# Optimization experiments

Measured on AMD Instinct MI355X. Metric: run time of the kernel, lower is better.

The kernel has to match this reference:

```python
import jax, jax.numpy as jnp
import numpy as np
import math

B, S, HID, L, NH, V, M = 8, 512, 768, 12, 12, 30522, 512
FF = 4 * HID
D = HID // NH


def sinusoidal_pe(seq_len, dim):
    pos = np.arange(seq_len, dtype=np.float32)[:, None]
    i = np.arange(dim // 2, dtype=np.float32)[None, :]
    ang = pos / np.power(10000.0, 2.0 * i / dim)
    pe = np.zeros((seq_len, dim), np.float32)
    pe[:, 0::2] = np.sin(ang)
    pe[:, 1::2] = np.cos(ang)
    return jnp.asarray(pe)


def setup_inputs() -> dict:
    key = jax.random.key(0)
    ks = iter(jax.random.split(key, 32))
    g = lambda sh: jax.random.normal(next(ks), sh, jnp.float32) * 0.02
    return {
        "token_ids": jax.random.randint(next(ks), (B, S), 0, V),
        "segment_info": jax.random.randint(next(ks), (B, S), 0, 2),
        "tok_emb": g((V, HID)),
        "seg_emb": g((3, HID)),
        "Wq": g((L, HID, HID)), "bq": jnp.zeros((L, HID)),
        "Wk": g((L, HID, HID)), "bk": jnp.zeros((L, HID)),
        "Wv": g((L, HID, HID)), "bv": jnp.zeros((L, HID)),
        "Wo": g((L, HID, HID)), "bo": jnp.zeros((L, HID)),
        "Wpk": g((L, HID, HID)),
        "Wpq": g((L, HID, HID)),
        "rel_emb": g((L, 2 * M, HID)),
        "ln1_g": jnp.ones((L, HID)), "ln1_b": jnp.zeros((L, HID)),
        "ln2_g": jnp.ones((L, HID)), "ln2_b": jnp.zeros((L, HID)),
        "W1": g((L, HID, FF)), "b1": jnp.zeros((L, FF)),
        "W2": g((L, FF, HID)), "b2": jnp.zeros((L, HID)),
        "lnf_g": jnp.ones((HID,)), "lnf_b": jnp.zeros((HID,)),
    }


def _ln(x, g, b):
    mu = x.mean(-1, keepdims=True)
    var = ((x - mu) ** 2).mean(-1, keepdims=True)
    return (x - mu) * jax.lax.rsqrt(var + 1e-5) * g + b


def _forward(token_ids, segment_info, tok_emb, seg_emb, layer_params, lnf_g, lnf_b):
    mask = token_ids != 0  # [B,S] valid-key mask
    x = tok_emb[token_ids] + sinusoidal_pe(S, HID)[None] + seg_emb[segment_info]
    qidx = jnp.arange(S)[:, None]
    # relative position bucket: clamp(q-k, -M, M-1) + M  -> [0, 2M)
    rel = jnp.clip(qidx - jnp.arange(S)[None, :], -M, M - 1) + M  # [S,S]
    scale = 1.0 / math.sqrt(3.0 * D)  # DeBERTa scales by sqrt(3d) for 3 score terms

    def body(x, p):
        (Wq, bq, Wk, bk, Wv, bv, Wo, bo, Wpk, Wpq, rel_e,
         l1g, l1b, l2g, l2b, W1, b1, W2, b2) = p
        # pre-norm attention sublayer
        h = _ln(x, l1g, l1b)
        q = (h @ Wq + bq).reshape(B, S, NH, D)
        k = (h @ Wk + bk).reshape(B, S, NH, D)
        v = (h @ Wv + bv).reshape(B, S, NH, D)
        c2c = jnp.einsum('bqhd,bkhd->bhqk', q, k)
        pk = (rel_e @ Wpk).reshape(2 * M, NH, D)
        pq = (rel_e @ Wpq).reshape(2 * M, NH, D)
        # content-to-position: Q_q . posK[rel(q,k)]
        c2p = jnp.einsum('bqhd,rhd->bhqr', q, pk)[:, :, qidx, rel]  # [B,NH,S,S]
        # position-to-content: K_k . posQ[rel(k,q)] -> gather over k rows then transpose
        p2c = jnp.einsum('bkhd,rhd->bhkr', k, pq)[:, :, qidx, rel]  # [B,NH,k,q]
        scores = (c2c + c2p + jnp.swapaxes(p2c, -1, -2)) * scale
        scores = jnp.where(mask[:, None, None, :], scores, -1e9)
        attn = jax.nn.softmax(scores, axis=-1)
        ctx = jnp.einsum('bhqk,bkhd->bqhd', attn, v).reshape(B, S, HID)
        x = x + ctx @ Wo + bo
        # pre-norm feedforward sublayer
        h2 = _ln(x, l2g, l2b)
        x = x + jax.nn.gelu(h2 @ W1 + b1, approximate=False) @ W2 + b2
        return x, None

    x, _ = jax.lax.scan(body, x, layer_params)
    return _ln(x, lnf_g, lnf_b)


def reference(token_ids, segment_info, tok_emb, seg_emb, Wq, bq, Wk, bk, Wv, bv,
              Wo, bo, Wpk, Wpq, rel_emb, ln1_g, ln1_b, ln2_g, ln2_b,
              W1, b1, W2, b2, lnf_g, lnf_b):
    lp = (Wq, bq, Wk, bk, Wv, bv, Wo, bo, Wpk, Wpq, rel_emb,
          ln1_g, ln1_b, ln2_g, ln2_b, W1, b1, W2, b2)
    return _forward(token_ids, segment_info, tok_emb, seg_emb, lp, lnf_g, lnf_b)
```

## Files before the change

### kernel.cpp

```cpp
#include <hip/hip_runtime.h>
#include <hip/hip_bf16.h>
#include <cstddef>
#include <cstdint>


constexpr int B   = 8;
constexpr int S   = 512;
constexpr int HID = 768;
constexpr int L   = 12;
constexpr int NH  = 12;
constexpr int D   = 64;
constexpr int FF  = 3072;
constexpr int M2  = 1024;
constexpr int NTOK = B * S;

using f32x4 = __attribute__((ext_vector_type(4))) float;
using s16x8 = __attribute__((ext_vector_type(8))) short;

__device__ inline float wave_sum(float v) {
#pragma unroll
  for (int o = 32; o > 0; o >>= 1) v += __shfl_xor(v, o, 64);
  return v;
}
__device__ inline unsigned short f2bf(float f) {
  __hip_bfloat16 h = __float2bfloat16(f);
  return *reinterpret_cast<unsigned short*>(&h);
}
__device__ inline float bf2f(unsigned short u) {
  union { unsigned int i; float f; } x;
  x.i = ((unsigned int)u) << 16;
  return x.f;
}
#define GLOAD16(gp, lp)                                                  \
  __builtin_amdgcn_global_load_lds(                                     \
      (const __attribute__((address_space(1))) void*)(gp),              \
      (__attribute__((address_space(3))) void*)(lp), 16, 0, 0)

__global__ void embed_kernel(const int* __restrict__ tok,
                             const int* __restrict__ seg,
                             const float* __restrict__ tok_emb,
                             const float* __restrict__ seg_emb,
                             float* __restrict__ x) {
  int row = blockIdx.x;
  int s = row & (S - 1);
  int t = tok[row];
  int sg = seg[row];
  for (int c = threadIdx.x; c < HID; c += blockDim.x) {
    int i = c >> 1;
    float ang = (float)s * powf(10000.0f, -2.0f * (float)i / (float)HID);
    float pe = (c & 1) ? cosf(ang) : sinf(ang);
    x[(size_t)row * HID + c] = tok_emb[(size_t)t * HID + c] + pe
                             + seg_emb[(size_t)sg * HID + c];
  }
}

template <int BF16OUT>
__global__ __launch_bounds__(256)
void ln_kernel(const float* __restrict__ in, void* __restrict__ outp,
               const float* __restrict__ g, const float* __restrict__ b,
               int nrows) {
  int wave = threadIdx.x >> 6, lane = threadIdx.x & 63;
  int row = blockIdx.x * 4 + wave;
  if (row >= nrows) return;
  const float* xr = in + (size_t)row * HID;
  float v[12];
  float s = 0.f;
#pragma unroll
  for (int i = 0; i < 12; i++) { v[i] = xr[lane + i * 64]; s += v[i]; }
  s = wave_sum(s);
  float mu = s * (1.0f / HID);
  float ss = 0.f;
#pragma unroll
  for (int i = 0; i < 12; i++) { float d = v[i] - mu; ss += d * d; }
  ss = wave_sum(ss);
  float inv = rsqrtf(ss * (1.0f / HID) + 1e-5f);
#pragma unroll
  for (int i = 0; i < 12; i++) {
    int c = lane + i * 64;
    float o = (v[i] - mu) * inv * g[c] + b[c];
    if (BF16OUT)
      ((unsigned short*)outp)[(size_t)row * HID + c] = f2bf(o);
    else
      ((float*)outp)[(size_t)row * HID + c] = o;
  }
}

__global__ __launch_bounds__(256)
void transpose_kernel(const float* __restrict__ src,
                      unsigned short* __restrict__ dst, int K, int N) {
  __shared__ float tile[32][33];
  int nt = blockIdx.x * 32, kt = blockIdx.y * 32;
  int tx = threadIdx.x & 31, ty = threadIdx.x >> 5;
#pragma unroll
  for (int i = 0; i < 4; i++)
    tile[ty + i * 8][tx] = src[(size_t)(kt + ty + i * 8) * N + nt + tx];
  __syncthreads();
#pragma unroll
  for (int i = 0; i < 4; i++)
    dst[(size_t)(nt + ty + i * 8) * K + kt + tx] = f2bf(tile[tx][ty + i * 8]);
}

__global__ __launch_bounds__(256)
void transpose6_kernel(const float* s0, const float* s1, const float* s2,
                       const float* s3, const float* s4, const float* s5,
                       unsigned short* __restrict__ dst) {
  const float* srcs[6] = {s0, s1, s2, s3, s4, s5};
  const float* src = srcs[blockIdx.z];
  unsigned short* d = dst + (size_t)blockIdx.z * HID * HID;
  __shared__ float tile[32][33];
  int nt = blockIdx.x * 32, kt = blockIdx.y * 32;
  int tx = threadIdx.x & 31, ty = threadIdx.x >> 5;
#pragma unroll
  for (int i = 0; i < 4; i++)
    tile[ty + i * 8][tx] = src[(size_t)(kt + ty + i * 8) * HID + nt + tx];
  __syncthreads();
#pragma unroll
  for (int i = 0; i < 4; i++)
    d[(size_t)(nt + ty + i * 8) * HID + kt + tx] = f2bf(tile[tx][ty + i * 8]);
}

__global__ void conv_bf16_kernel(const float* __restrict__ src,
                                 unsigned short* __restrict__ dst, int n) {
  int i = blockIdx.x * 256 + threadIdx.x;
  if (i < n) dst[i] = f2bf(src[i]);
}

__global__ void concat_bias(const float* __restrict__ bq,
                            const float* __restrict__ bk,
                            const float* __restrict__ bv,
                            float* __restrict__ bqkv) {
  int i = blockIdx.x * 256 + threadIdx.x;
  if (i >= L * 2304) return;
  int l = i / 2304, c = i % 2304;
  float v = (c < 768) ? bq[l * 768 + c]
          : (c < 1536) ? bk[l * 768 + c - 768] : bv[l * 768 + c - 1536];
  bqkv[i] = v;
}

template <int TN, int OUT_BF16, int GELU, int PARTIAL>
__global__ __launch_bounds__(256)
void mfma_gemm(const unsigned short* __restrict__ A,
               const unsigned short* __restrict__ Bt,
               const float* __restrict__ bias, const float* __restrict__ res,
               void* __restrict__ C, int Mr, int K, int N, int Kc) {
  constexpr int NW = TN / 32;
  __shared__ unsigned short As[128 * 32];
  __shared__ unsigned short Bs[TN * 32];
  int t = threadIdx.x, wave = t >> 6, lane = t & 63;
  int r0 = blockIdx.y * 128, n0 = blockIdx.x * TN;
  int kb = blockIdx.z * Kc;
  int wr = (wave >> 1) * 64;
  int wc = (wave & 1) * (TN / 2);

  f32x4 acc[4][NW] = {};
  int srow = lane >> 2, selem = (lane & 3) * 8;

  for (int k0 = kb; k0 < kb + Kc; k0 += 32) {
    __syncthreads();
    {
      const unsigned short* gA =
          A + (size_t)(r0 + wave * 32 + srow) * K + k0 + selem;
      unsigned short* lA = &As[(wave * 32) * 32];
      GLOAD16(gA, lA);
      GLOAD16(gA + (size_t)16 * K, lA + 16 * 32);
      if (TN == 128) {
        const unsigned short* gB =
            Bt + (size_t)(n0 + wave * 32 + srow) * K + k0 + selem;
        unsigned short* lB = &Bs[(wave * 32) * 32];
        GLOAD16(gB, lB);
        GLOAD16(gB + (size_t)16 * K, lB + 16 * 32);
      } else {
        const unsigned short* gB =
            Bt + (size_t)(n0 + wave * 16 + srow) * K + k0 + selem;
        GLOAD16(gB, &Bs[(wave * 16) * 32]);
      }
    }
    __syncthreads();

    s16x8 af[4], bf[NW];
#pragma unroll
    for (int m = 0; m < 4; m++)
      af[m] = *(const s16x8*)&As[(wr + m * 16 + (lane & 15)) * 32 + (lane >> 4) * 8];
#pragma unroll
    for (int n = 0; n < NW; n++)
      bf[n] = *(const s16x8*)&Bs[(wc + n * 16 + (lane & 15)) * 32 + (lane >> 4) * 8];
#pragma unroll
    for (int m = 0; m < 4; m++)
#pragma unroll
      for (int n = 0; n < NW; n++)
        acc[m][n] = __builtin_amdgcn_mfma_f32_16x16x32_bf16(af[m], bf[n],
                                                            acc[m][n], 0, 0, 0);
  }

  if (PARTIAL) {
    float* Cp = (float*)C + (size_t)blockIdx.z * Mr * N;
#pragma unroll
    for (int n = 0; n < NW; n++) {
      int c = n0 + wc + n * 16 + (lane & 15);
#pragma unroll
      for (int m = 0; m < 4; m++) {
        int rb = r0 + wr + m * 16 + ((lane >> 4) << 2);
#pragma unroll
        for (int j = 0; j < 4; j++)
          Cp[(size_t)(rb + j) * N + c] = acc[m][n][j];
      }
    }
    return;
  }
#pragma unroll
  for (int n = 0; n < NW; n++) {
    int c = n0 + wc + n * 16 + (lane & 15);
    float bv = bias ? bias[c] : 0.f;
#pragma unroll
    for (int m = 0; m < 4; m++) {
      int rb = r0 + wr + m * 16 + ((lane >> 4) << 2);
#pragma unroll
      for (int j = 0; j < 4; j++) {
        int r = rb + j;
        float val = acc[m][n][j] + bv;
        if (GELU) val = 0.5f * val * (1.0f + erff(val * 0.70710678118654752f));
        if (res)  val += res[(size_t)r * N + c];
        if (OUT_BF16)
          ((unsigned short*)C)[(size_t)r * N + c] = f2bf(val);
        else
          ((float*)C)[(size_t)r * N + c] = val;
      }
    }
  }
}

template <int LAST>
__global__ __launch_bounds__(256)
void combine_ln(const float* __restrict__ part,
                float* __restrict__ x, const float* __restrict__ bias,
                const float* __restrict__ g, const float* __restrict__ bb,
                void* __restrict__ outp) {
  int row = blockIdx.x, t = threadIdx.x;
  int wave = t >> 6, lane = t & 63;
  __shared__ float red[4];
  float v[3];
  float s = 0.f;
#pragma unroll
  for (int i = 0; i < 3; i++) {
    int c = t + i * 256;
    size_t idx = (size_t)row * HID + c;
    float val = x[idx] + part[idx] + part[(size_t)NTOK * HID + idx] + bias[c];
    if (!LAST) x[idx] = val;
    v[i] = val;
    s += val;
  }
  s = wave_sum(s);
  if (lane == 0) red[wave] = s;
  __syncthreads();
  float mu = (red[0] + red[1] + red[2] + red[3]) * (1.0f / HID);
  float ss = 0.f;
#pragma unroll
  for (int i = 0; i < 3; i++) { float d = v[i] - mu; ss += d * d; }
  ss = wave_sum(ss);
  __syncthreads();
  if (lane == 0) red[wave] = ss;
  __syncthreads();
  float inv = rsqrtf((red[0] + red[1] + red[2] + red[3]) * (1.0f / HID) + 1e-5f);
#pragma unroll
  for (int i = 0; i < 3; i++) {
    int c = t + i * 256;
    float o = (v[i] - mu) * inv * g[c] + bb[c];
    if (LAST)
      ((float*)outp)[(size_t)row * HID + c] = o;
    else
      ((unsigned short*)outp)[(size_t)row * HID + c] = f2bf(o);
  }
}

__global__ __launch_bounds__(256)
void transpose_v(const unsigned short* __restrict__ qkv,
                 unsigned short* __restrict__ vt) {
  __shared__ unsigned short tile[32][34];
  int bh = blockIdx.z;
  int b = bh / NH, h = bh % NH;
  int s0 = blockIdx.x * 32, d0 = blockIdx.y * 32;
  int tx = threadIdx.x & 31, ty = threadIdx.x >> 5;
#pragma unroll
  for (int i = 0; i < 4; i++)
    tile[ty + i * 8][tx] =
        qkv[(size_t)(b * S + s0 + ty + i * 8) * 2304 + 1536 + h * 64 + d0 + tx];
  __syncthreads();
#pragma unroll
  for (int i = 0; i < 4; i++)
    vt[((size_t)bh * 64 + d0 + ty + i * 8) * S + s0 + tx] = tile[tx][ty + i * 8];
}

__global__ __launch_bounds__(256)
void flash_attn(const unsigned short* __restrict__ qkv,
                const unsigned short* __restrict__ pkq,
                const unsigned short* __restrict__ vt,
                const int* __restrict__ tok,
                unsigned short* __restrict__ ctx) {
  constexpr int RS = 72, TS = 130;
  __shared__ unsigned short Qs[64 * RS];
  __shared__ unsigned short KPs[64 * RS];
  __shared__ unsigned short Vs[64 * RS];
  __shared__ unsigned short Band[2 * 128 * RS];
  __shared__ int smTok[64];
  unsigned short* PKb = Band;
  unsigned short* PQb = Band + 128 * RS;
  unsigned short* c2pL = Band;
  unsigned short* p2cL = Band + 64 * TS;

  int t = threadIdx.x, wave = t >> 6, lane = t & 63;
  int bh = blockIdx.y;
  int b = bh / NH, h = bh % NH;
  int q0 = blockIdx.x * 64;
  int l15 = lane & 15, l4 = lane >> 4;

#pragma unroll
  for (int i = 0; i < 2; i++) {
    int c = t + i * 256;
    int r = c >> 3, d0 = (c & 7) * 8;
    *(s16x8*)&Qs[r * RS + d0] =
        *(const s16x8*)&qkv[(size_t)(b * S + q0 + r) * 2304 + h * 64 + d0];
  }

  float m[4], l[4];
  f32x4 accO[4];
#pragma unroll
  for (int j = 0; j < 4; j++) { m[j] = -1e30f; l[j] = 0.f; }
#pragma unroll
  for (int n = 0; n < 4; n++) accO[n] = (f32x4){0.f, 0.f, 0.f, 0.f};

  const float scale = 0.07216878364870323f;

  for (int k0 = 0; k0 < S; k0 += 64) {
#pragma unroll
    for (int i = 0; i < 2; i++) {
      int c = t + i * 256;
      int r = c >> 3, d0 = (c & 7) * 8;
      *(s16x8*)&KPs[r * RS + d0] =
          *(const s16x8*)&qkv[(size_t)(b * S + k0 + r) * 2304 + 768 + h * 64 + d0];
      *(s16x8*)&Vs[r * RS + d0] =
          *(const s16x8*)&vt[((size_t)bh * 64 + r) * S + k0 + d0];
    }
    int lo1 = q0 - k0 + 449;
    int lo2 = k0 - q0 + 449;
#pragma unroll
    for (int i = 0; i < 4; i++) {
      int c = t + i * 256;
      int tt = c >> 3, d0 = (c & 7) * 8;
      int r1 = lo1 + tt; r1 = r1 < 0 ? 0 : (r1 > M2 - 1 ? M2 - 1 : r1);
      int r2 = lo2 + tt; r2 = r2 < 0 ? 0 : (r2 > M2 - 1 ? M2 - 1 : r2);
      *(s16x8*)&PKb[tt * RS + d0] = *(const s16x8*)&pkq[(size_t)r1 * 1536 + h * 64 + d0];
      *(s16x8*)&PQb[tt * RS + d0] =
          *(const s16x8*)&pkq[(size_t)r2 * 1536 + 768 + h * 64 + d0];
    }
    if (t < 64) smTok[t] = tok[b * S + k0 + t];
    __syncthreads();

    f32x4 c2c[4] = {};
    f32x4 cp[8] = {}, pc[8] = {};
#pragma unroll
    for (int ks = 0; ks < 2; ks++) {
      int koff = ks * 32 + l4 * 8;
      s16x8 aq = *(const s16x8*)&Qs[(wave * 16 + l15) * RS + koff];
      s16x8 ak = *(const s16x8*)&KPs[(wave * 16 + l15) * RS + koff];
#pragma unroll
      for (int n = 0; n < 4; n++) {
        s16x8 bk = *(const s16x8*)&KPs[(n * 16 + l15) * RS + koff];
        c2c[n] = __builtin_amdgcn_mfma_f32_16x16x32_bf16(aq, bk, c2c[n], 0, 0, 0);
      }
#pragma unroll
      for (int tt = 0; tt < 8; tt++) {
        s16x8 bpk = *(const s16x8*)&PKb[(tt * 16 + l15) * RS + koff];
        s16x8 bpq = *(const s16x8*)&PQb[(tt * 16 + l15) * RS + koff];
        cp[tt] = __builtin_amdgcn_mfma_f32_16x16x32_bf16(aq, bpk, cp[tt], 0, 0, 0);
        pc[tt] = __builtin_amdgcn_mfma_f32_16x16x32_bf16(ak, bpq, pc[tt], 0, 0, 0);
      }
    }
    __syncthreads();

    {
      int rw = wave * 16 + (l4 << 2);
#pragma unroll
      for (int tt = 0; tt < 8; tt++)
#pragma unroll
        for (int j = 0; j < 4; j++) {
          c2pL[(rw + j) * TS + tt * 16 + l15] = f2bf(cp[tt][j]);
          p2cL[(rw + j) * TS + tt * 16 + l15] = f2bf(pc[tt][j]);
        }
    }
    __syncthreads();

    float p[4][4];
    float rmax[4];
#pragma unroll
    for (int j = 0; j < 4; j++) rmax[j] = -1e30f;
#pragma unroll
    for (int n = 0; n < 4; n++) {
      int ik = n * 16 + l15;
      bool msk = (smTok[ik] == 0);
#pragma unroll
      for (int j = 0; j < 4; j++) {
        int iq = wave * 16 + (l4 << 2) + j;
        float sc = c2c[n][j]
                 + bf2f(c2pL[iq * TS + (iq - ik + 63)])
                 + bf2f(p2cL[ik * TS + (ik - iq + 63)]);
        sc *= scale;
        if (msk) sc = -1e9f;
        p[n][j] = sc;
        rmax[j] = fmaxf(rmax[j], sc);
      }
    }
#pragma unroll
    for (int o = 8; o > 0; o >>= 1)
#pragma unroll
      for (int j = 0; j < 4; j++)
        rmax[j] = fmaxf(rmax[j], __shfl_xor(rmax[j], o, 64));
    float al[4];
#pragma unroll
    for (int j = 0; j < 4; j++) {
      float mn = fmaxf(m[j], rmax[j]);
      al[j] = __expf(m[j] - mn);
      m[j] = mn;
    }
    float rs[4] = {0.f, 0.f, 0.f, 0.f};
#pragma unroll
    for (int n = 0; n < 4; n++)
#pragma unroll
      for (int j = 0; j < 4; j++) {
        p[n][j] = __expf(p[n][j] - m[j]);
        rs[j] += p[n][j];
      }
#pragma unroll
    for (int o = 8; o > 0; o >>= 1)
#pragma unroll
      for (int j = 0; j < 4; j++) rs[j] += __shfl_xor(rs[j], o, 64);
#pragma unroll
    for (int j = 0; j < 4; j++) l[j] = l[j] * al[j] + rs[j];
#pragma unroll
    for (int n = 0; n < 4; n++)
#pragma unroll
      for (int j = 0; j < 4; j++) accO[n][j] *= al[j];

    {
      int rw = wave * 16 + (l4 << 2);
#pragma unroll
      for (int n = 0; n < 4; n++)
#pragma unroll
        for (int j = 0; j < 4; j++)
          KPs[(rw + j) * RS + n * 16 + l15] = f2bf(p[n][j]);
    }
    __syncthreads();

#pragma unroll
    for (int ks = 0; ks < 2; ks++) {
      int koff = ks * 32 + l4 * 8;
      s16x8 ap = *(const s16x8*)&KPs[(wave * 16 + l15) * RS + koff];
#pragma unroll
      for (int n = 0; n < 4; n++) {
        s16x8 bv2 = *(const s16x8*)&Vs[(n * 16 + l15) * RS + koff];
        accO[n] = __builtin_amdgcn_mfma_f32_16x16x32_bf16(ap, bv2, accO[n], 0, 0, 0);
      }
    }
    __syncthreads();
  }

#pragma unroll
  for (int n = 0; n < 4; n++) {
    int dd = h * 64 + n * 16 + l15;
#pragma unroll
    for (int j = 0; j < 4; j++) {
      int iq = q0 + wave * 16 + (l4 << 2) + j;
      ctx[(size_t)(b * S + iq) * HID + dd] = f2bf(accO[n][j] / l[j]);
    }
  }
}

extern "C" void kernel_launch(void* const* d_in, const int* in_sizes, int n_in,
                              void* d_out, int out_size, void* d_ws,
                              size_t ws_size, hipStream_t stream) {
  (void)in_sizes; (void)n_in; (void)out_size; (void)ws_size;
  const int*   tok     = (const int*)d_in[0];
  const int*   seg     = (const int*)d_in[1];
  const float* tok_emb = (const float*)d_in[2];
  const float* seg_emb = (const float*)d_in[3];
  const float* Wq  = (const float*)d_in[4];
  const float* bq  = (const float*)d_in[5];
  const float* Wk  = (const float*)d_in[6];
  const float* bk  = (const float*)d_in[7];
  const float* Wv  = (const float*)d_in[8];
  const float* bv  = (const float*)d_in[9];
  const float* Wo  = (const float*)d_in[10];
  const float* bo  = (const float*)d_in[11];
  const float* Wpk = (const float*)d_in[12];
  const float* Wpq = (const float*)d_in[13];
  const float* rel = (const float*)d_in[14];
  const float* ln1g = (const float*)d_in[15];
  const float* ln1b = (const float*)d_in[16];
  const float* ln2g = (const float*)d_in[17];
  const float* ln2b = (const float*)d_in[18];
  const float* W1  = (const float*)d_in[19];
  const float* b1  = (const float*)d_in[20];
  const float* W2  = (const float*)d_in[21];
  const float* b2  = (const float*)d_in[22];
  const float* lnfg = (const float*)d_in[23];
  const float* lnfb = (const float*)d_in[24];
  float* out = (float*)d_out;

  char* base = (char*)d_ws;
  size_t off = 0;
  auto alloc = [&](size_t bytes) -> void* {
    void* p = base + off;
    off += (bytes + 255) & ~(size_t)255;
    return p;
  };
  const size_t XSZ = (size_t)NTOK * HID;
  float* x = (float*)alloc(XSZ * 4);
  unsigned short* qkv16 = (unsigned short*)alloc((size_t)NTOK * 2304 * 2);
  unsigned short* pkq16 = (unsigned short*)alloc((size_t)M2 * 1536 * 2);
  unsigned short* vt16  = (unsigned short*)alloc(XSZ * 2);
  unsigned short* act16 = (unsigned short*)alloc(XSZ * 2);
  unsigned short* ff16  = (unsigned short*)alloc((size_t)NTOK * FF * 2);
  unsigned short* rel16 = (unsigned short*)alloc((size_t)M2 * HID * 2);
  unsigned short* wt6   = (unsigned short*)alloc((size_t)6 * HID * HID * 2);
  unsigned short* wt1   = (unsigned short*)alloc((size_t)HID * FF * 2);
  unsigned short* wt2   = (unsigned short*)alloc((size_t)HID * FF * 2);
  float* skbuf = (float*)alloc((size_t)2 * NTOK * HID * 4);
  float* bqkv  = (float*)alloc((size_t)L * 2304 * 4);

  const size_t WSQ = (size_t)HID * HID;

  embed_kernel<<<NTOK, 256, 0, stream>>>(tok, seg, tok_emb, seg_emb, x);
  concat_bias<<<(L * 2304 + 255) / 256, 256, 0, stream>>>(bq, bk, bv, bqkv);
  ln_kernel<1><<<NTOK / 4, 256, 0, stream>>>(x, act16, ln1g, ln1b, NTOK);

  for (int l = 0; l < L; l++) {
    transpose6_kernel<<<dim3(HID / 32, HID / 32, 6), 256, 0, stream>>>(
        Wq + l * WSQ, Wk + l * WSQ, Wv + l * WSQ, Wo + l * WSQ,
        Wpk + l * WSQ, Wpq + l * WSQ, wt6);
    transpose_kernel<<<dim3(FF / 32, HID / 32), 256, 0, stream>>>(
        W1 + (size_t)l * HID * FF, wt1, HID, FF);
    transpose_kernel<<<dim3(HID / 32, FF / 32), 256, 0, stream>>>(
        W2 + (size_t)l * FF * HID, wt2, FF, HID);
    conv_bf16_kernel<<<(M2 * HID + 255) / 256, 256, 0, stream>>>(
        rel + (size_t)l * M2 * HID, rel16, M2 * HID);

    mfma_gemm<128, 1, 0, 0><<<dim3(2304 / 128, NTOK / 128, 1), 256, 0, stream>>>(
        act16, wt6, bqkv + l * 2304, nullptr, qkv16, NTOK, HID, 2304, HID);
    mfma_gemm<64, 1, 0, 0><<<dim3(1536 / 64, M2 / 128, 1), 256, 0, stream>>>(
        rel16, wt6 + 4 * WSQ, nullptr, nullptr, pkq16, M2, HID, 1536, HID);
    transpose_v<<<dim3(S / 32, D / 32, B * NH), 256, 0, stream>>>(qkv16, vt16);
    flash_attn<<<dim3(S / 64, B * NH), 256, 0, stream>>>(
        qkv16, pkq16, vt16, tok, act16);
    mfma_gemm<64, 0, 0, 0><<<dim3(HID / 64, NTOK / 128, 1), 256, 0, stream>>>(
        act16, wt6 + 3 * WSQ, bo + l * HID, x, x, NTOK, HID, HID, HID);

    ln_kernel<1><<<NTOK / 4, 256, 0, stream>>>(x, act16, ln2g + l * HID,
                                               ln2b + l * HID, NTOK);
    mfma_gemm<128, 1, 1, 0><<<dim3(FF / 128, NTOK / 128, 1), 256, 0, stream>>>(
        act16, wt1, b1 + l * FF, nullptr, ff16, NTOK, HID, FF, HID);
    mfma_gemm<64, 0, 0, 1><<<dim3(HID / 64, NTOK / 128, 2), 256, 0, stream>>>(
        ff16, wt2, nullptr, nullptr, skbuf, NTOK, FF, HID, FF / 2);
    if (l < L - 1) {
      combine_ln<0><<<NTOK, 256, 0, stream>>>(
          skbuf, x, b2 + l * HID, ln1g + (l + 1) * HID, ln1b + (l + 1) * HID,
          act16);
    } else {
      combine_ln<1><<<NTOK, 256, 0, stream>>>(
          skbuf, x, b2 + l * HID, lnfg, lnfb, out);
    }
  }
}
```

Before: 3.967 ms.

## Prefetch next KV/position tiles in registers and keep Q fragments resident in flash attention

New measurement: 4.048 ms. +2.0%, slower.

```diff
diff --git a/kernel.cpp b/kernel.cpp
--- a/kernel.cpp
+++ b/kernel.cpp
@@ -86,21 +86,6 @@
 }
 
 __global__ __launch_bounds__(256)
-void transpose_kernel(const float* __restrict__ src,
-                      unsigned short* __restrict__ dst, int K, int N) {
-  __shared__ float tile[32][33];
-  int nt = blockIdx.x * 32, kt = blockIdx.y * 32;
-  int tx = threadIdx.x & 31, ty = threadIdx.x >> 5;
-#pragma unroll
-  for (int i = 0; i < 4; i++)
-    tile[ty + i * 8][tx] = src[(size_t)(kt + ty + i * 8) * N + nt + tx];
-  __syncthreads();
-#pragma unroll
-  for (int i = 0; i < 4; i++)
-    dst[(size_t)(nt + ty + i * 8) * K + kt + tx] = f2bf(tile[tx][ty + i * 8]);
-}
-
-__global__ __launch_bounds__(256)
 void transpose6_kernel(const float* s0, const float* s1, const float* s2,
                        const float* s3, const float* s4, const float* s5,
                        unsigned short* __restrict__ dst) {
@@ -117,6 +102,27 @@
 #pragma unroll
   for (int i = 0; i < 4; i++)
     d[(size_t)(nt + ty + i * 8) * HID + kt + tx] = f2bf(tile[tx][ty + i * 8]);
+}
+
+__global__ __launch_bounds__(256)
+void transpose_ff(const float* __restrict__ W1s, const float* __restrict__ W2s,
+                  unsigned short* __restrict__ d1, unsigned short* __restrict__ d2) {
+  const float* src = blockIdx.z ? W2s : W1s;
+  unsigned short* dst = blockIdx.z ? d2 : d1;
+  int K = blockIdx.z ? FF : HID;
+  int N = blockIdx.z ? HID : FF;
+  int nt, kt;
+  if (blockIdx.z) { nt = blockIdx.y * 32; kt = blockIdx.x * 32; }
+  else            { nt = blockIdx.x * 32; kt = blockIdx.y * 32; }
+  __shared__ float tile[32][33];
+  int tx = threadIdx.x & 31, ty = threadIdx.x >> 5;
+#pragma unroll
+  for (int i = 0; i < 4; i++)
+    tile[ty + i * 8][tx] = src[(size_t)(kt + ty + i * 8) * N + nt + tx];
+  __syncthreads();
+#pragma unroll
+  for (int i = 0; i < 4; i++)
+    dst[(size_t)(nt + ty + i * 8) * K + kt + tx] = f2bf(tile[tx][ty + i * 8]);
 }
 
 __global__ void conv_bf16_kernel(const float* __restrict__ src,
@@ -297,7 +303,6 @@
                 const int* __restrict__ tok,
                 unsigned short* __restrict__ ctx) {
   constexpr int RS = 72, TS = 130;
-  __shared__ unsigned short Qs[64 * RS];
   __shared__ unsigned short KPs[64 * RS];
   __shared__ unsigned short Vs[64 * RS];
   __shared__ unsigned short Band[2 * 128 * RS];
@@ -305,87 +310,123 @@
   unsigned short* PKb = Band;
   unsigned short* PQb = Band + 128 * RS;
   unsigned short* c2pL = Band;
-  unsigned short* p2cL = Band + 64 * TS;
+  unsigned short* p2cL = Band + 128 * RS;
 
   int t = threadIdx.x, wave = t >> 6, lane = t & 63;
   int bh = blockIdx.y;
   int b = bh / NH, h = bh % NH;
   int q0 = blockIdx.x * 64;
   int l15 = lane & 15, l4 = lane >> 4;
-
-#pragma unroll
-  for (int i = 0; i < 2; i++) {
-    int c = t + i * 256;
-    int r = c >> 3, d0 = (c & 7) * 8;
-    *(s16x8*)&Qs[r * RS + d0] =
-        *(const s16x8*)&qkv[(size_t)(b * S + q0 + r) * 2304 + h * 64 + d0];
-  }
-
-  float m[4], l[4];
+  const float scale = 0.07216878364870323f;
+
+  int sr0 = t >> 3, sd0 = (t & 7) * 8;
+  int sr1 = sr0 + 32;
+
+  s16x8 qf[4][2];
+#pragma unroll
+  for (int m = 0; m < 4; m++)
+#pragma unroll
+    for (int ks = 0; ks < 2; ks++)
+      qf[m][ks] = *(const s16x8*)&qkv[(size_t)(b * S + q0 + m * 16 + l15) * 2304
+                                      + h * 64 + ks * 32 + l4 * 8];
+
+  float mrow[4], lrow[4];
   f32x4 accO[4];
 #pragma unroll
-  for (int j = 0; j < 4; j++) { m[j] = -1e30f; l[j] = 0.f; }
+  for (int j = 0; j < 4; j++) { mrow[j] = -1e30f; lrow[j] = 0.f; }
 #pragma unroll
   for (int n = 0; n < 4; n++) accO[n] = (f32x4){0.f, 0.f, 0.f, 0.f};
 
-  const float scale = 0.07216878364870323f;
-
-  for (int k0 = 0; k0 < S; k0 += 64) {
-#pragma unroll
-    for (int i = 0; i < 2; i++) {
-      int c = t + i * 256;
-      int r = c >> 3, d0 = (c & 7) * 8;
-      *(s16x8*)&KPs[r * RS + d0] =
-          *(const s16x8*)&qkv[(size_t)(b * S + k0 + r) * 2304 + 768 + h * 64 + d0];
-      *(s16x8*)&Vs[r * RS + d0] =
-          *(const s16x8*)&vt[((size_t)bh * 64 + r) * S + k0 + d0];
-    }
-    int lo1 = q0 - k0 + 449;
-    int lo2 = k0 - q0 + 449;
+  {
+    *(s16x8*)&KPs[sr0 * RS + sd0] =
+        *(const s16x8*)&qkv[(size_t)(b * S + sr0) * 2304 + 768 + h * 64 + sd0];
+    *(s16x8*)&KPs[sr1 * RS + sd0] =
+        *(const s16x8*)&qkv[(size_t)(b * S + sr1) * 2304 + 768 + h * 64 + sd0];
+    *(s16x8*)&Vs[sr0 * RS + sd0] =
+        *(const s16x8*)&vt[((size_t)bh * 64 + sr0) * S + sd0];
+    *(s16x8*)&Vs[sr1 * RS + sd0] =
+        *(const s16x8*)&vt[((size_t)bh * 64 + sr1) * S + sd0];
+    int lo1 = q0 + 449, lo2 = -q0 + 449;
 #pragma unroll
     for (int i = 0; i < 4; i++) {
-      int c = t + i * 256;
-      int tt = c >> 3, d0 = (c & 7) * 8;
+      int tt = sr0 + i * 32;
       int r1 = lo1 + tt; r1 = r1 < 0 ? 0 : (r1 > M2 - 1 ? M2 - 1 : r1);
       int r2 = lo2 + tt; r2 = r2 < 0 ? 0 : (r2 > M2 - 1 ? M2 - 1 : r2);
-      *(s16x8*)&PKb[tt * RS + d0] = *(const s16x8*)&pkq[(size_t)r1 * 1536 + h * 64 + d0];
-      *(s16x8*)&PQb[tt * RS + d0] =
-          *(const s16x8*)&pkq[(size_t)r2 * 1536 + 768 + h * 64 + d0];
-    }
-    if (t < 64) smTok[t] = tok[b * S + k0 + t];
+      *(s16x8*)&PKb[tt * RS + sd0] =
+          *(const s16x8*)&pkq[(size_t)r1 * 1536 + h * 64 + sd0];
+      *(s16x8*)&PQb[tt * RS + sd0] =
+          *(const s16x8*)&pkq[(size_t)r2 * 1536 + 768 + h * 64 + sd0];
+    }
+    if (t < 64) smTok[t] = tok[b * S + t];
+  }
+  __syncthreads();
+
+  for (int k0 = 0; k0 < S; k0 += 64) {
+    int k0n = k0 + 64;
+    bool pfv = (k0n < S);
+
+    s16x8 pfK0, pfK1, pfV0, pfV1, pfPK[4], pfPQ[4];
+    int pfTok = 0;
+    if (pfv) {
+      pfK0 = *(const s16x8*)&qkv[(size_t)(b * S + k0n + sr0) * 2304 + 768 + h * 64 + sd0];
+      pfK1 = *(const s16x8*)&qkv[(size_t)(b * S + k0n + sr1) * 2304 + 768 + h * 64 + sd0];
+      pfV0 = *(const s16x8*)&vt[((size_t)bh * 64 + sr0) * S + k0n + sd0];
+      pfV1 = *(const s16x8*)&vt[((size_t)bh * 64 + sr1) * S + k0n + sd0];
+      int lo1 = q0 - k0n + 449, lo2 = k0n - q0 + 449;
+#pragma unroll
+      for (int i = 0; i < 4; i++) {
+        int tt = sr0 + i * 32;
+        int r1 = lo1 + tt; r1 = r1 < 0 ? 0 : (r1 > M2 - 1 ? M2 - 1 : r1);
+        int r2 = lo2 + tt; r2 = r2 < 0 ? 0 : (r2 > M2 - 1 ? M2 - 1 : r2);
+        pfPK[i] = *(const s16x8*)&pkq[(size_t)r1 * 1536 + h * 64 + sd0];
+        pfPQ[i] = *(const s16x8*)&pkq[(size_t)r2 * 1536 + 768 + h * 64 + sd0];
+      }
+      if (t < 64) pfTok = tok[b * S + k0n + t];
+    }
+
+    s16x8 kf[4][2];
+#pragma unroll
+    for (int m = 0; m < 4; m++)
+#pragma unroll
+      for (int ks = 0; ks < 2; ks++)
+        kf[m][ks] = *(const s16x8*)&KPs[(m * 16 + l15) * RS + ks * 32 + l4 * 8];
+
+    f32x4 c2c[4] = {};
+    f32x4 cp[4][2] = {}, pc[4][2] = {};
+    __builtin_amdgcn_s_setprio(1);
+#pragma unroll
+    for (int ks = 0; ks < 2; ks++) {
+#pragma unroll
+      for (int n = 0; n < 4; n++)
+        c2c[n] = __builtin_amdgcn_mfma_f32_16x16x32_bf16(qf[wave][ks], kf[n][ks],
+                                                         c2c[n], 0, 0, 0);
+#pragma unroll
+      for (int u = 0; u < 2; u++) {
+        s16x8 bpk = *(const s16x8*)&PKb[(wave * 32 + u * 16 + l15) * RS + ks * 32 + l4 * 8];
+        s16x8 bpq = *(const s16x8*)&PQb[(wave * 32 + u * 16 + l15) * RS + ks * 32 + l4 * 8];
+#pragma unroll
+        for (int m = 0; m < 4; m++) {
+          cp[m][u] = __builtin_amdgcn_mfma_f32_16x16x32_bf16(qf[m][ks], bpk,
+                                                             cp[m][u], 0, 0, 0);
+          pc[m][u] = __builtin_amdgcn_mfma_f32_16x16x32_bf16(kf[m][ks], bpq,
+                                                             pc[m][u], 0, 0, 0);
+        }
+      }
+    }
+    __builtin_amdgcn_s_setprio(0);
     __syncthreads();
 
-    f32x4 c2c[4] = {};
-    f32x4 cp[8] = {}, pc[8] = {};
-#pragma unroll
-    for (int ks = 0; ks < 2; ks++) {
-      int koff = ks * 32 + l4 * 8;
-      s16x8 aq = *(const s16x8*)&Qs[(wave * 16 + l15) * RS + koff];
-      s16x8 ak = *(const s16x8*)&KPs[(wave * 16 + l15) * RS + koff];
-#pragma unroll
-      for (int n = 0; n < 4; n++) {
-        s16x8 bk = *(const s16x8*)&KPs[(n * 16 + l15) * RS + koff];
-        c2c[n] = __builtin_amdgcn_mfma_f32_16x16x32_bf16(aq, bk, c2c[n], 0, 0, 0);
-      }
-#pragma unroll
-      for (int tt = 0; tt < 8; tt++) {
-        s16x8 bpk = *(const s16x8*)&PKb[(tt * 16 + l15) * RS + koff];
-        s16x8 bpq = *(const s16x8*)&PQb[(tt * 16 + l15) * RS + koff];
-        cp[tt] = __builtin_amdgcn_mfma_f32_16x16x32_bf16(aq, bpk, cp[tt], 0, 0, 0);
-        pc[tt] = __builtin_amdgcn_mfma_f32_16x16x32_bf16(ak, bpq, pc[tt], 0, 0, 0);
-      }
-    }
-    __syncthreads();
-
     {
-      int rw = wave * 16 + (l4 << 2);
-#pragma unroll
-      for (int tt = 0; tt < 8; tt++)
-#pragma unroll
-        for (int j = 0; j < 4; j++) {
-          c2pL[(rw + j) * TS + tt * 16 + l15] = f2bf(cp[tt][j]);
-          p2cL[(rw + j) * TS + tt * 16 + l15] = f2bf(pc[tt][j]);
-        }
+      int rw = l4 << 2;
+#pragma unroll
+      for (int m = 0; m < 4; m++)
+#pragma unroll
+        for (int u = 0; u < 2; u++)
+#pragma unroll
+          for (int j = 0; j < 4; j++) {
+            c2pL[(m * 16 + rw + j) * TS + wave * 32 + u * 16 + l15] = f2bf(cp[m][u][j]);
+            p2cL[(m * 16 + rw + j) * TS + wave * 32 + u * 16 + l15] = f2bf(pc[m][u][j]);
+          }
     }
     __syncthreads();
 
@@ -417,16 +458,16 @@
     float al[4];
 #pragma unroll
     for (int j = 0; j < 4; j++) {
-      float mn = fmaxf(m[j], rmax[j]);
-      al[j] = __expf(m[j] - mn);
-      m[j] = mn;
+      float mn = fmaxf(mrow[j], rmax[j]);
+      al[j] = __expf(mrow[j] - mn);
+      mrow[j] = mn;
     }
     float rs[4] = {0.f, 0.f, 0.f, 0.f};
 #pragma unroll
     for (int n = 0; n < 4; n++)
 #pragma unroll
       for (int j = 0; j < 4; j++) {
-        p[n][j] = __expf(p[n][j] - m[j]);
+        p[n][j] = __expf(p[n][j] - mrow[j]);
         rs[j] += p[n][j];
       }
 #pragma unroll
@@ -434,7 +475,7 @@
 #pragma unroll
       for (int j = 0; j < 4; j++) rs[j] += __shfl_xor(rs[j], o, 64);
 #pragma unroll
-    for (int j = 0; j < 4; j++) l[j] = l[j] * al[j] + rs[j];
+    for (int j = 0; j < 4; j++) lrow[j] = lrow[j] * al[j] + rs[j];
 #pragma unroll
     for (int n = 0; n < 4; n++)
 #pragma unroll
@@ -450,6 +491,7 @@
     }
     __syncthreads();
 
+    __builtin_amdgcn_s_setprio(1);
 #pragma unroll
     for (int ks = 0; ks < 2; ks++) {
       int koff = ks * 32 + l4 * 8;
@@ -460,6 +502,22 @@
         accO[n] = __builtin_amdgcn_mfma_f32_16x16x32_bf16(ap, bv2, accO[n], 0, 0, 0);
       }
     }
+    __builtin_amdgcn_s_setprio(0);
+    __syncthreads();
+
+    if (pfv) {
+      *(s16x8*)&KPs[sr0 * RS + sd0] = pfK0;
+      *(s16x8*)&KPs[sr1 * RS + sd0] = pfK1;
+      *(s16x8*)&Vs[sr0 * RS + sd0] = pfV0;
+      *(s16x8*)&Vs[sr1 * RS + sd0] = pfV1;
+#pragma unroll
+      for (int i = 0; i < 4; i++) {
+        int tt = sr0 + i * 32;
+        *(s16x8*)&PKb[tt * RS + sd0] = pfPK[i];
+        *(s16x8*)&PQb[tt * RS + sd0] = pfPQ[i];
+      }
+      if (t < 64) smTok[t] = pfTok;
+    }
     __syncthreads();
   }
 
@@ -469,7 +527,7 @@
 #pragma unroll
     for (int j = 0; j < 4; j++) {
       int iq = q0 + wave * 16 + (l4 << 2) + j;
-      ctx[(size_t)(b * S + iq) * HID + dd] = f2bf(accO[n][j] / l[j]);
+      ctx[(size_t)(b * S + iq) * HID + dd] = f2bf(accO[n][j] / lrow[j]);
     }
   }
 }
@@ -536,10 +594,8 @@
     transpose6_kernel<<<dim3(HID / 32, HID / 32, 6), 256, 0, stream>>>(
         Wq + l * WSQ, Wk + l * WSQ, Wv + l * WSQ, Wo + l * WSQ,
         Wpk + l * WSQ, Wpq + l * WSQ, wt6);
-    transpose_kernel<<<dim3(FF / 32, HID / 32), 256, 0, stream>>>(
-        W1 + (size_t)l * HID * FF, wt1, HID, FF);
-    transpose_kernel<<<dim3(HID / 32, FF / 32), 256, 0, stream>>>(
-        W2 + (size_t)l * FF * HID, wt2, FF, HID);
+    transpose_ff<<<dim3(FF / 32, HID / 32, 2), 256, 0, stream>>>(
+        W1 + (size_t)l * HID * FF, W2 + (size_t)l * FF * HID, wt1, wt2);
     conv_bf16_kernel<<<(M2 * HID + 255) / 256, 256, 0, stream>>>(
         rel + (size_t)l * M2 * HID, rel16, M2 * HID);
 
```

## Split attention over key range with flash-decoding combine, merge FF transposes

Applied to the files above, without the earlier changes.

After: 4.021 ms. About the same (+1.4%).

```diff
diff --git a/kernel.cpp b/kernel.cpp
--- a/kernel.cpp
+++ b/kernel.cpp
@@ -86,21 +86,6 @@
 }
 
 __global__ __launch_bounds__(256)
-void transpose_kernel(const float* __restrict__ src,
-                      unsigned short* __restrict__ dst, int K, int N) {
-  __shared__ float tile[32][33];
-  int nt = blockIdx.x * 32, kt = blockIdx.y * 32;
-  int tx = threadIdx.x & 31, ty = threadIdx.x >> 5;
-#pragma unroll
-  for (int i = 0; i < 4; i++)
-    tile[ty + i * 8][tx] = src[(size_t)(kt + ty + i * 8) * N + nt + tx];
-  __syncthreads();
-#pragma unroll
-  for (int i = 0; i < 4; i++)
-    dst[(size_t)(nt + ty + i * 8) * K + kt + tx] = f2bf(tile[tx][ty + i * 8]);
-}
-
-__global__ __launch_bounds__(256)
 void transpose6_kernel(const float* s0, const float* s1, const float* s2,
                        const float* s3, const float* s4, const float* s5,
                        unsigned short* __restrict__ dst) {
@@ -117,6 +102,27 @@
 #pragma unroll
   for (int i = 0; i < 4; i++)
     d[(size_t)(nt + ty + i * 8) * HID + kt + tx] = f2bf(tile[tx][ty + i * 8]);
+}
+
+__global__ __launch_bounds__(256)
+void transpose_ff(const float* __restrict__ W1s, const float* __restrict__ W2s,
+                  unsigned short* __restrict__ d1, unsigned short* __restrict__ d2) {
+  const float* src = blockIdx.z ? W2s : W1s;
+  unsigned short* dst = blockIdx.z ? d2 : d1;
+  int K = blockIdx.z ? FF : HID;
+  int N = blockIdx.z ? HID : FF;
+  int nt, kt;
+  if (blockIdx.z) { nt = blockIdx.y * 32; kt = blockIdx.x * 32; }
+  else            { nt = blockIdx.x * 32; kt = blockIdx.y * 32; }
+  __shared__ float tile[32][33];
+  int tx = threadIdx.x & 31, ty = threadIdx.x >> 5;
+#pragma unroll
+  for (int i = 0; i < 4; i++)
+    tile[ty + i * 8][tx] = src[(size_t)(kt + ty + i * 8) * N + nt + tx];
+  __syncthreads();
+#pragma unroll
+  for (int i = 0; i < 4; i++)
+    dst[(size_t)(nt + ty + i * 8) * K + kt + tx] = f2bf(tile[tx][ty + i * 8]);
 }
 
 __global__ void conv_bf16_kernel(const float* __restrict__ src,
@@ -295,7 +301,8 @@
                 const unsigned short* __restrict__ pkq,
                 const unsigned short* __restrict__ vt,
                 const int* __restrict__ tok,
-                unsigned short* __restrict__ ctx) {
+                float* __restrict__ pO,
+                float* __restrict__ pML) {
   constexpr int RS = 72, TS = 130;
   __shared__ unsigned short Qs[64 * RS];
   __shared__ unsigned short KPs[64 * RS];
@@ -311,6 +318,7 @@
   int bh = blockIdx.y;
   int b = bh / NH, h = bh % NH;
   int q0 = blockIdx.x * 64;
+  int kr0 = blockIdx.z * 256;
   int l15 = lane & 15, l4 = lane >> 4;
 
 #pragma unroll
@@ -330,7 +338,7 @@
 
   const float scale = 0.07216878364870323f;
 
-  for (int k0 = 0; k0 < S; k0 += 64) {
+  for (int k0 = kr0; k0 < kr0 + 256; k0 += 64) {
 #pragma unroll
     for (int i = 0; i < 2; i++) {
       int c = t + i * 256;
@@ -348,7 +356,8 @@
       int tt = c >> 3, d0 = (c & 7) * 8;
       int r1 = lo1 + tt; r1 = r1 < 0 ? 0 : (r1 > M2 - 1 ? M2 - 1 : r1);
       int r2 = lo2 + tt; r2 = r2 < 0 ? 0 : (r2 > M2 - 1 ? M2 - 1 : r2);
-      *(s16x8*)&PKb[tt * RS + d0] = *(const s16x8*)&pkq[(size_t)r1 * 1536 + h * 64 + d0];
+      *(s16x8*)&PKb[tt * RS + d0] =
+          *(const s16x8*)&pkq[(size_t)r1 * 1536 + h * 64 + d0];
       *(s16x8*)&PQb[tt * RS + d0] =
           *(const s16x8*)&pkq[(size_t)r2 * 1536 + 768 + h * 64 + d0];
     }
@@ -463,14 +472,51 @@
     __syncthreads();
   }
 
+  int pb = bh * 8 + blockIdx.x;
+  float* Ob = pO + (((size_t)pb * 2 + blockIdx.z) << 12);
 #pragma unroll
   for (int n = 0; n < 4; n++) {
-    int dd = h * 64 + n * 16 + l15;
 #pragma unroll
     for (int j = 0; j < 4; j++) {
-      int iq = q0 + wave * 16 + (l4 << 2) + j;
-      ctx[(size_t)(b * S + iq) * HID + dd] = f2bf(accO[n][j] / l[j]);
-    }
+      int row = wave * 16 + (l4 << 2) + j;
+      Ob[row * 64 + n * 16 + l15] = accO[n][j];
+    }
+  }
+  if (l15 == 0) {
+    float* mlb = pML + ((size_t)pb * 2 + blockIdx.z) * 128;
+#pragma unroll
+    for (int j = 0; j < 4; j++) {
+      int row = wave * 16 + (l4 << 2) + j;
+      mlb[row] = m[j];
+      mlb[64 + row] = l[j];
+    }
+  }
+}
+
+__global__ __launch_bounds__(256)
+void flash_combine(const float* __restrict__ pO, const float* __restrict__ pML,
+                   unsigned short* __restrict__ ctx) {
+  int pb = blockIdx.x;
+  int bh = pb >> 3, qt = pb & 7;
+  int b = bh / NH, h = bh % NH;
+  int t = threadIdx.x;
+  int r = t >> 2, c0 = (t & 3) * 16;
+  const float* ml = pML + (size_t)pb * 256;
+  float m1 = ml[r], l1 = ml[64 + r];
+  float m2 = ml[128 + r], l2 = ml[192 + r];
+  float M = fmaxf(m1, m2);
+  float a1 = __expf(m1 - M), a2 = __expf(m2 - M);
+  float linv = 1.0f / (a1 * l1 + a2 * l2);
+  const float* O1 = pO + ((size_t)pb * 2) * 4096 + r * 64 + c0;
+  const float* O2 = O1 + 4096;
+  unsigned short* o = ctx + (size_t)(b * S + qt * 64 + r) * HID + h * 64 + c0;
+#pragma unroll
+  for (int i = 0; i < 4; i++) {
+    f32x4 v1 = *(const f32x4*)&O1[i * 4];
+    f32x4 v2 = *(const f32x4*)&O2[i * 4];
+#pragma unroll
+    for (int j = 0; j < 4; j++)
+      o[i * 4 + j] = f2bf((a1 * v1[j] + a2 * v2[j]) * linv);
   }
 }
 
@@ -526,6 +572,9 @@
   float* skbuf = (float*)alloc((size_t)2 * NTOK * HID * 4);
   float* bqkv  = (float*)alloc((size_t)L * 2304 * 4);
 
+  float* pO  = skbuf;
+  float* pML = (float*)ff16;
+
   const size_t WSQ = (size_t)HID * HID;
 
   embed_kernel<<<NTOK, 256, 0, stream>>>(tok, seg, tok_emb, seg_emb, x);
@@ -536,10 +585,8 @@
     transpose6_kernel<<<dim3(HID / 32, HID / 32, 6), 256, 0, stream>>>(
         Wq + l * WSQ, Wk + l * WSQ, Wv + l * WSQ, Wo + l * WSQ,
         Wpk + l * WSQ, Wpq + l * WSQ, wt6);
-    transpose_kernel<<<dim3(FF / 32, HID / 32), 256, 0, stream>>>(
-        W1 + (size_t)l * HID * FF, wt1, HID, FF);
-    transpose_kernel<<<dim3(HID / 32, FF / 32), 256, 0, stream>>>(
-        W2 + (size_t)l * FF * HID, wt2, FF, HID);
+    transpose_ff<<<dim3(FF / 32, HID / 32, 2), 256, 0, stream>>>(
+        W1 + (size_t)l * HID * FF, W2 + (size_t)l * FF * HID, wt1, wt2);
     conv_bf16_kernel<<<(M2 * HID + 255) / 256, 256, 0, stream>>>(
         rel + (size_t)l * M2 * HID, rel16, M2 * HID);
 
@@ -548,8 +595,9 @@
     mfma_gemm<64, 1, 0, 0><<<dim3(1536 / 64, M2 / 128, 1), 256, 0, stream>>>(
         rel16, wt6 + 4 * WSQ, nullptr, nullptr, pkq16, M2, HID, 1536, HID);
     transpose_v<<<dim3(S / 32, D / 32, B * NH), 256, 0, stream>>>(qkv16, vt16);
-    flash_attn<<<dim3(S / 64, B * NH), 256, 0, stream>>>(
-        qkv16, pkq16, vt16, tok, act16);
+    flash_attn<<<dim3(S / 64, B * NH, 2), 256, 0, stream>>>(
+        qkv16, pkq16, vt16, tok, pO, pML);
+    flash_combine<<<B * NH * (S / 64), 256, 0, stream>>>(pO, pML, act16);
     mfma_gemm<64, 0, 0, 0><<<dim3(HID / 64, NTOK / 128, 1), 256, 0, stream>>>(
         act16, wt6 + 3 * WSQ, bo + l * HID, x, x, NTOK, HID, HID, HID);
 
```

## Read positional bands and Q directly from global in attention; merge FF transposes

Applied to the files above, without the earlier changes.

New measurement: 4.694 ms. 18.3% more time.

```diff
diff --git a/kernel.cpp b/kernel.cpp
--- a/kernel.cpp
+++ b/kernel.cpp
@@ -86,21 +86,6 @@
 }
 
 __global__ __launch_bounds__(256)
-void transpose_kernel(const float* __restrict__ src,
-                      unsigned short* __restrict__ dst, int K, int N) {
-  __shared__ float tile[32][33];
-  int nt = blockIdx.x * 32, kt = blockIdx.y * 32;
-  int tx = threadIdx.x & 31, ty = threadIdx.x >> 5;
-#pragma unroll
-  for (int i = 0; i < 4; i++)
-    tile[ty + i * 8][tx] = src[(size_t)(kt + ty + i * 8) * N + nt + tx];
-  __syncthreads();
-#pragma unroll
-  for (int i = 0; i < 4; i++)
-    dst[(size_t)(nt + ty + i * 8) * K + kt + tx] = f2bf(tile[tx][ty + i * 8]);
-}
-
-__global__ __launch_bounds__(256)
 void transpose6_kernel(const float* s0, const float* s1, const float* s2,
                        const float* s3, const float* s4, const float* s5,
                        unsigned short* __restrict__ dst) {
@@ -117,6 +102,27 @@
 #pragma unroll
   for (int i = 0; i < 4; i++)
     d[(size_t)(nt + ty + i * 8) * HID + kt + tx] = f2bf(tile[tx][ty + i * 8]);
+}
+
+__global__ __launch_bounds__(256)
+void transpose_ff(const float* __restrict__ W1s, const float* __restrict__ W2s,
+                  unsigned short* __restrict__ d1, unsigned short* __restrict__ d2) {
+  const float* src = blockIdx.z ? W2s : W1s;
+  unsigned short* dst = blockIdx.z ? d2 : d1;
+  int K = blockIdx.z ? FF : HID;
+  int N = blockIdx.z ? HID : FF;
+  int nt, kt;
+  if (blockIdx.z) { nt = blockIdx.y * 32; kt = blockIdx.x * 32; }
+  else            { nt = blockIdx.x * 32; kt = blockIdx.y * 32; }
+  __shared__ float tile[32][33];
+  int tx = threadIdx.x & 31, ty = threadIdx.x >> 5;
+#pragma unroll
+  for (int i = 0; i < 4; i++)
+    tile[ty + i * 8][tx] = src[(size_t)(kt + ty + i * 8) * N + nt + tx];
+  __syncthreads();
+#pragma unroll
+  for (int i = 0; i < 4; i++)
+    dst[(size_t)(nt + ty + i * 8) * K + kt + tx] = f2bf(tile[tx][ty + i * 8]);
 }
 
 __global__ void conv_bf16_kernel(const float* __restrict__ src,
@@ -297,29 +303,23 @@
                 const int* __restrict__ tok,
                 unsigned short* __restrict__ ctx) {
   constexpr int RS = 72, TS = 130;
-  __shared__ unsigned short Qs[64 * RS];
   __shared__ unsigned short KPs[64 * RS];
   __shared__ unsigned short Vs[64 * RS];
-  __shared__ unsigned short Band[2 * 128 * RS];
-  __shared__ int smTok[64];
-  unsigned short* PKb = Band;
-  unsigned short* PQb = Band + 128 * RS;
-  unsigned short* c2pL = Band;
-  unsigned short* p2cL = Band + 64 * TS;
+  __shared__ unsigned short c2pL[64 * TS];
+  __shared__ unsigned short p2cL[64 * TS];
 
   int t = threadIdx.x, wave = t >> 6, lane = t & 63;
   int bh = blockIdx.y;
   int b = bh / NH, h = bh % NH;
   int q0 = blockIdx.x * 64;
   int l15 = lane & 15, l4 = lane >> 4;
-
-#pragma unroll
-  for (int i = 0; i < 2; i++) {
-    int c = t + i * 256;
-    int r = c >> 3, d0 = (c & 7) * 8;
-    *(s16x8*)&Qs[r * RS + d0] =
-        *(const s16x8*)&qkv[(size_t)(b * S + q0 + r) * 2304 + h * 64 + d0];
-  }
+  const float scale = 0.07216878364870323f;
+
+  s16x8 qf[2];
+#pragma unroll
+  for (int ks = 0; ks < 2; ks++)
+    qf[ks] = *(const s16x8*)&qkv[(size_t)(b * S + q0 + wave * 16 + l15) * 2304
+                                 + h * 64 + ks * 32 + l4 * 8];
 
   float m[4], l[4];
   f32x4 accO[4];
@@ -327,8 +327,6 @@
   for (int j = 0; j < 4; j++) { m[j] = -1e30f; l[j] = 0.f; }
 #pragma unroll
   for (int n = 0; n < 4; n++) accO[n] = (f32x4){0.f, 0.f, 0.f, 0.f};
-
-  const float scale = 0.07216878364870323f;
 
   for (int k0 = 0; k0 < S; k0 += 64) {
 #pragma unroll
@@ -340,27 +338,16 @@
       *(s16x8*)&Vs[r * RS + d0] =
           *(const s16x8*)&vt[((size_t)bh * 64 + r) * S + k0 + d0];
     }
+    __syncthreads();
+
     int lo1 = q0 - k0 + 449;
     int lo2 = k0 - q0 + 449;
-#pragma unroll
-    for (int i = 0; i < 4; i++) {
-      int c = t + i * 256;
-      int tt = c >> 3, d0 = (c & 7) * 8;
-      int r1 = lo1 + tt; r1 = r1 < 0 ? 0 : (r1 > M2 - 1 ? M2 - 1 : r1);
-      int r2 = lo2 + tt; r2 = r2 < 0 ? 0 : (r2 > M2 - 1 ? M2 - 1 : r2);
-      *(s16x8*)&PKb[tt * RS + d0] = *(const s16x8*)&pkq[(size_t)r1 * 1536 + h * 64 + d0];
-      *(s16x8*)&PQb[tt * RS + d0] =
-          *(const s16x8*)&pkq[(size_t)r2 * 1536 + 768 + h * 64 + d0];
-    }
-    if (t < 64) smTok[t] = tok[b * S + k0 + t];
-    __syncthreads();
-
     f32x4 c2c[4] = {};
     f32x4 cp[8] = {}, pc[8] = {};
 #pragma unroll
     for (int ks = 0; ks < 2; ks++) {
       int koff = ks * 32 + l4 * 8;
-      s16x8 aq = *(const s16x8*)&Qs[(wave * 16 + l15) * RS + koff];
+      s16x8 aq = qf[ks];
       s16x8 ak = *(const s16x8*)&KPs[(wave * 16 + l15) * RS + koff];
 #pragma unroll
       for (int n = 0; n < 4; n++) {
@@ -369,13 +356,15 @@
       }
 #pragma unroll
       for (int tt = 0; tt < 8; tt++) {
-        s16x8 bpk = *(const s16x8*)&PKb[(tt * 16 + l15) * RS + koff];
-        s16x8 bpq = *(const s16x8*)&PQb[(tt * 16 + l15) * RS + koff];
+        int rr = tt * 16 + l15;
+        int r1 = lo1 + rr; r1 = r1 < 0 ? 0 : (r1 > M2 - 1 ? M2 - 1 : r1);
+        int r2 = lo2 + rr; r2 = r2 < 0 ? 0 : (r2 > M2 - 1 ? M2 - 1 : r2);
+        s16x8 bpk = *(const s16x8*)&pkq[(size_t)r1 * 1536 + h * 64 + koff];
+        s16x8 bpq = *(const s16x8*)&pkq[(size_t)r2 * 1536 + 768 + h * 64 + koff];
         cp[tt] = __builtin_amdgcn_mfma_f32_16x16x32_bf16(aq, bpk, cp[tt], 0, 0, 0);
         pc[tt] = __builtin_amdgcn_mfma_f32_16x16x32_bf16(ak, bpq, pc[tt], 0, 0, 0);
       }
     }
-    __syncthreads();
 
     {
       int rw = wave * 16 + (l4 << 2);
@@ -396,7 +385,7 @@
 #pragma unroll
     for (int n = 0; n < 4; n++) {
       int ik = n * 16 + l15;
-      bool msk = (smTok[ik] == 0);
+      bool msk = (tok[b * S + k0 + ik] == 0);
 #pragma unroll
       for (int j = 0; j < 4; j++) {
         int iq = wave * 16 + (l4 << 2) + j;
@@ -536,10 +525,8 @@
     transpose6_kernel<<<dim3(HID / 32, HID / 32, 6), 256, 0, stream>>>(
         Wq + l * WSQ, Wk + l * WSQ, Wv + l * WSQ, Wo + l * WSQ,
         Wpk + l * WSQ, Wpq + l * WSQ, wt6);
-    transpose_kernel<<<dim3(FF / 32, HID / 32), 256, 0, stream>>>(
-        W1 + (size_t)l * HID * FF, wt1, HID, FF);
-    transpose_kernel<<<dim3(HID / 32, FF / 32), 256, 0, stream>>>(
-        W2 + (size_t)l * FF * HID, wt2, FF, HID);
+    transpose_ff<<<dim3(FF / 32, HID / 32, 2), 256, 0, stream>>>(
+        W1 + (size_t)l * HID * FF, W2 + (size_t)l * FF * HID, wt1, wt2);
     conv_bf16_kernel<<<(M2 * HID + 255) / 256, 256, 0, stream>>>(
         rel + (size_t)l * M2 * HID, rel16, M2 * HID);
 
```
